# Performance work log

Hardware: AMD Instinct MI355X
Metric: run time of the kernel (lower is better)

Reference implementation:

```python
import jax, jax.numpy as jnp
import numpy as np
import math

T = 32
DIM = 1024
BATCH = 4096
ETA = 1.0


def setup_inputs() -> dict:
    key = jax.random.key(0)
    k1, k2, k3, k4 = jax.random.split(key, 4)
    x = jax.random.normal(k1, (BATCH, DIM), dtype=jnp.float32)
    mu = jax.random.uniform(k2, (T, DIM), dtype=jnp.float32, minval=-0.5, maxval=0.5)
    rho = jax.random.uniform(k3, (T, DIM), dtype=jnp.float32, minval=-0.5, maxval=0.5)
    # stochastic Beta(gamma_1, gamma_2) draws in the original (scipy beta.rvs);
    # passed as an explicit input, kept strictly inside (0, 1)
    beta_samples = jax.random.uniform(k4, (BATCH, T), dtype=jnp.float32,
                                      minval=0.01, maxval=0.99)
    return {"x": x, "mu": mu, "rho": rho, "beta_samples": beta_samples}


def _forward(x, mu, rho, beta_samples):
    B, D = x.shape
    Tn = mu.shape[0]
    log2pi = math.log(2.0 * math.pi)

    std = jnp.log1p(jnp.exp(rho))              # [T, D]
    log_std_sum = jnp.sum(jnp.log(std), axis=-1)   # [T]
    inv_var = 1.0 / (std * std)                # [T, D]

    # Diagonal Gaussian log-prob, batched over all T components via GEMMs
    quad = (jnp.einsum('bd,td->bt', x * x, inv_var)
            - 2.0 * jnp.einsum('bd,td->bt', x, mu * inv_var)
            + jnp.sum(mu * mu * inv_var, axis=-1)[None, :])   # [B, T]
    log_pdfs = -0.5 * D * log2pi - log_std_sum[None, :] - 0.5 * quad  # [B, T]

    # entropy of each diagonal Gaussian, broadcast to batch
    entropy = (D / 2.0) * (log2pi + 1.0) + log_std_sum   # [T]
    entropy = jnp.broadcast_to(entropy[None, :], (B, Tn))

    # stick-breaking weights: pi = mix_weights(beta)[:, :-1]
    beta1m_cumprod = jnp.cumprod(1.0 - beta_samples, axis=-1)   # [B, T]
    pi = beta_samples * jnp.concatenate(
        [jnp.ones((B, 1), x.dtype), beta1m_cumprod[:, :-1]], axis=-1)  # [B, T]
    log_pi = jnp.log(pi)

    # get_phi
    kl_gaussian = log_pdfs + entropy            # [B, T]
    N_t_gaussian = jnp.sum(kl_gaussian, axis=0, keepdims=True)  # [1, T]
    N_t_pi = jnp.sum(log_pi, axis=0, keepdims=True)             # [1, T]
    mix = N_t_pi / (N_t_gaussian + N_t_pi)      # [1, T]
    kl = mix * kl_gaussian + (1.0 - mix) * log_pi
    phi_new = jax.nn.softmax(kl, axis=1)        # [B, T]
    kl_g_mixed = mix * kl_gaussian              # [B, T]

    likelihood = jnp.mean(jnp.sum(phi_new * kl_g_mixed, axis=1), axis=0)  # scalar
    return likelihood


def reference(x, mu, rho, beta_samples):
    return _forward(x, mu, rho, beta_samples)
```

## Files before the change

kernel.cpp:

```cpp
#include <hip/hip_runtime.h>
#include <math.h>

constexpr int NT = 32;
constexpr int ND = 1024;
constexpr int NB = 4096;
constexpr int ROWS = 16;
constexpr int NBLK_MAIN = NB / ROWS;

typedef float f2 __attribute__((ext_vector_type(2)));

constexpr int OFF_M2C = 32768;
constexpr int OFF_C2  = 65536;
constexpr int OFF_KLG = 65600;
constexpr int OFF_LPI = 196672;
constexpr int OFF_PG  = 327744;
constexpr int OFF_PP  = 335936;

__global__ __launch_bounds__(256) void k_stats(const float* __restrict__ mu,
                                               const float* __restrict__ rho,
                                               float* __restrict__ ws,
                                               float* __restrict__ out) {
  float* ivc = ws;
  float* m2c = ws + OFF_M2C;
  float* c2  = ws + OFF_C2;

  const int t = blockIdx.x;
  const int c = threadIdx.x;

  float4 mu4  = reinterpret_cast<const float4*>(mu  + t * ND)[c];
  float4 rho4 = reinterpret_cast<const float4*>(rho + t * ND)[c];

  float rr[4] = {rho4.x, rho4.y, rho4.z, rho4.w};
  float mm[4] = {mu4.x,  mu4.y,  mu4.z,  mu4.w};
  float iv[4], m2[4];
  float c2p = 0.0f;
#pragma unroll
  for (int j = 0; j < 4; ++j) {
    float sd  = log1pf(expf(rr[j]));
    float ivv = 1.0f / (sd * sd);
    iv[j] = ivv;
    m2[j] = -2.0f * mm[j] * ivv;
    c2p  += mm[j] * mm[j] * ivv;
  }
  float4 iv4 = {iv[0], iv[1], iv[2], iv[3]};
  float4 m24 = {m2[0], m2[1], m2[2], m2[3]};
  reinterpret_cast<float4*>(ivc)[c * NT + t] = iv4;
  reinterpret_cast<float4*>(m2c)[c * NT + t] = m24;

#pragma unroll
  for (int m = 32; m >= 1; m >>= 1) c2p += __shfl_xor(c2p, m, 64);
  __shared__ float red[4];
  const int wave = threadIdx.x >> 6, lane = threadIdx.x & 63;
  if (lane == 0) red[wave] = c2p;
  __syncthreads();
  if (threadIdx.x == 0) {
    c2[t] = red[0] + red[1] + red[2] + red[3];
    if (t == 0) out[0] = 0.0f;
  }
}

__global__ __launch_bounds__(1024, 4) void k_main(const float* __restrict__ x,
                                                  const float* __restrict__ beta,
                                                  float* __restrict__ ws) {
  const float* ivc = ws;
  const float* m2c = ws + OFF_M2C;
  const float* c2  = ws + OFF_C2;
  float* klg = ws + OFF_KLG;
  float* lpi = ws + OFF_LPI;
  float* Pg  = ws + OFF_PG;
  float* Pp  = ws + OFF_PP;

  const int tid  = threadIdx.x;
  const int q    = tid >> 6;
  const int lane = tid & 63;
  const int h = lane >> 5, t = lane & 31;
  const int row0 = blockIdx.x * ROWS;

  __shared__ float xs[ROWS * ND];
  __shared__ float part[16][ROWS][32];

  {
    const float4* xg4 = reinterpret_cast<const float4*>(x) + (size_t)row0 * 256;
    float4* xs4w = reinterpret_cast<float4*>(xs);
#pragma unroll
    for (int k = 0; k < 4; ++k) {
      xs4w[k * 1024 + tid] = xg4[k * 1024 + tid];
    }
  }
  __syncthreads();

  const int c0 = q * 16 + h * 8;
  const float4* ivp = reinterpret_cast<const float4*>(ivc) + (size_t)c0 * NT + t;
  const float4* m2p = reinterpret_cast<const float4*>(m2c) + (size_t)c0 * NT + t;
  const float4* xs4 = reinterpret_cast<const float4*>(xs) + c0;

  f2 a2[ROWS];
#pragma unroll
  for (int r = 0; r < ROWS; ++r) a2[r] = (f2){0.f, 0.f};

#pragma unroll 1
  for (int i = 0; i < 8; ++i) {
    float4 iv4 = ivp[(size_t)i * NT];
    float4 m24 = m2p[(size_t)i * NT];
    const f2 ivl = {iv4.x, iv4.y}, ivh = {iv4.z, iv4.w};
    const f2 ml  = {m24.x, m24.y}, mh  = {m24.z, m24.w};
#pragma unroll
    for (int r = 0; r < ROWS; ++r) {
      float4 xv = xs4[r * 256 + i];
      const f2 xl = {xv.x, xv.y}, xh = {xv.z, xv.w};
      a2[r] = __builtin_elementwise_fma(xl, __builtin_elementwise_fma(xl, ivl, ml), a2[r]);
      a2[r] = __builtin_elementwise_fma(xh, __builtin_elementwise_fma(xh, ivh, mh), a2[r]);
    }
  }
#pragma unroll
  for (int r = 0; r < ROWS; ++r) {
    float s = a2[r].x + a2[r].y;
    s += __shfl_xor(s, 32, 64);
    if (h == 0) part[q][r][t] = s;
  }
  __syncthreads();

  const int rr = tid >> 5, t2 = tid & 31;
  float kv = 0.f, lp = 0.f;
  if (tid < 512) {
    float quad = 0.f;
#pragma unroll
    for (int w = 0; w < 16; ++w) quad += part[w][rr][t2];
    kv = 512.0f - 0.5f * (quad + c2[t2]);
    klg[(size_t)(row0 + rr) * NT + t2] = kv;

    const float b = beta[(size_t)(row0 + rr) * NT + t2];
    const float l1m = log1pf(-b);
    float s = l1m;
#pragma unroll
    for (int d = 1; d < 32; d <<= 1) {
      float v = __shfl_up(s, (unsigned)d, 32);
      if (t2 >= d) s += v;
    }
    lp = logf(b) + (s - l1m);
    lpi[(size_t)(row0 + rr) * NT + t2] = lp;
  }
  __syncthreads();
  if (tid < 512) {
    part[0][rr][t2] = kv;
    part[1][rr][t2] = lp;
  }
  __syncthreads();
  if (tid < 32) {
    float sg = 0.f, sp = 0.f;
#pragma unroll
    for (int r = 0; r < ROWS; ++r) { sg += part[0][r][tid]; sp += part[1][r][tid]; }
    Pg[(size_t)blockIdx.x * NT + tid] = sg;
    Pp[(size_t)blockIdx.x * NT + tid] = sp;
  }
}

__global__ __launch_bounds__(512) void k_final(const float* __restrict__ ws,
                                               float* __restrict__ out) {
  const float* klg = ws + OFF_KLG;
  const float* lpi = ws + OFF_LPI;
  const float* Pg  = ws + OFF_PG;
  const float* Pp  = ws + OFF_PP;

  const int tid  = threadIdx.x;
  const int wave = tid >> 6, lane = tid & 63;
  const int t = tid & 31;
  const int g = tid >> 5;

  __shared__ float ngF[32], npF[32];
  __shared__ float redG[8][32], redP[8][32];
  __shared__ float red[8];

  {
    float sg = 0.f, sp = 0.f;
#pragma unroll 4
    for (int b = g; b < NBLK_MAIN; b += 16) {
      sg += Pg[(size_t)b * NT + t];
      sp += Pp[(size_t)b * NT + t];
    }
    sg += __shfl_xor(sg, 32, 64);
    sp += __shfl_xor(sp, 32, 64);
    if (lane < 32) { redG[wave][t] = sg; redP[wave][t] = sp; }
  }
  __syncthreads();
  if (tid < 32) {
    float ng = 0.f, np = 0.f;
#pragma unroll
    for (int w = 0; w < 8; ++w) { ng += redG[w][tid]; np += redP[w][tid]; }
    ngF[tid] = ng;
    npF[tid] = np;
  }
  __syncthreads();

  const int row = blockIdx.x * 16 + g;
  const float kg = klg[(size_t)row * NT + t];
  const float lp = lpi[(size_t)row * NT + t];
  const float ng = ngF[t], np = npF[t];
  const float mix  = np / (ng + np);
  const float klgm = mix * kg;
  const float kl   = klgm + (1.0f - mix) * lp;

  float m = kl;
#pragma unroll
  for (int mk = 16; mk >= 1; mk >>= 1) m = fmaxf(m, __shfl_xor(m, mk, 64));
  const float e = expf(kl - m);
  float num = e * klgm, den = e;
#pragma unroll
  for (int mk = 16; mk >= 1; mk >>= 1) {
    num += __shfl_xor(num, mk, 64);
    den += __shfl_xor(den, mk, 64);
  }
  float s = num / den;
  s += __shfl_xor(s, 32, 64);

  if (lane == 0) red[wave] = s;
  __syncthreads();
  if (tid == 0) {
    float tot = 0.f;
#pragma unroll
    for (int w = 0; w < 8; ++w) tot += red[w];
    atomicAdd(out, tot * (1.0f / (float)NB));
  }
}

extern "C" void kernel_launch(void* const* d_in, const int* in_sizes, int n_in,
                              void* d_out, int out_size, void* d_ws, size_t ws_size,
                              hipStream_t stream) {
  const float* x    = (const float*)d_in[0];
  const float* mu   = (const float*)d_in[1];
  const float* rho  = (const float*)d_in[2];
  const float* beta = (const float*)d_in[3];
  float* out = (float*)d_out;
  float* ws  = (float*)d_ws;

  hipLaunchKernelGGL(k_stats, dim3(32),        dim3(256),  0, stream, mu, rho, ws, out);
  hipLaunchKernelGGL(k_main,  dim3(NBLK_MAIN), dim3(1024), 0, stream, x, beta, ws);
  hipLaunchKernelGGL(k_final, dim3(256),       dim3(512),  0, stream, ws, out);
}
```

Before: 29.63 us.

## Split main kernel rows into two tiles with register-staged prefetch of next tile

The main kernel now uses 512 threads and processes 16 rows as two 8-row tiles. The second tile's x data is loaded into registers while the first tile is computed, then written to a second shared buffer, so global loads overlap compute. Each wave now covers 32 columns instead of 16, giving fewer cross-wave partials but more serial work per thread. Per-tile partial sums double, so the final reduction reads twice as many partials. The extra barriers and the serialised epilogues between tiles may offset the overlap gain.

```diff
diff --git a/kernel.cpp b/kernel.cpp
--- a/kernel.cpp
+++ b/kernel.cpp
@@ -4,8 +4,10 @@
 constexpr int NT = 32;
 constexpr int ND = 1024;
 constexpr int NB = 4096;
-constexpr int ROWS = 16;
-constexpr int NBLK_MAIN = NB / ROWS;
+constexpr int TROWS = 8;
+constexpr int NTILE = 2;
+constexpr int NBLK_MAIN = NB / (TROWS * NTILE);
+constexpr int NPART = NB / TROWS;
 
 typedef float f2 __attribute__((ext_vector_type(2)));
 
@@ -14,7 +16,7 @@
 constexpr int OFF_KLG = 65600;
 constexpr int OFF_LPI = 196672;
 constexpr int OFF_PG  = 327744;
-constexpr int OFF_PP  = 335936;
+constexpr int OFF_PP  = 344128;
 
 __global__ __launch_bounds__(256) void k_stats(const float* __restrict__ mu,
                                                const float* __restrict__ rho,
@@ -59,9 +61,88 @@
   }
 }
 
-__global__ __launch_bounds__(1024, 4) void k_main(const float* __restrict__ x,
-                                                  const float* __restrict__ beta,
-                                                  float* __restrict__ ws) {
+__device__ __forceinline__ void compute_tile(const float* __restrict__ xsb,
+                                             const float* __restrict__ ivc,
+                                             const float* __restrict__ m2c,
+                                             float (*part)[8][32],
+                                             int q, int h, int t) {
+  const int c0 = q * 32 + h * 16;
+  const float4* ivp = reinterpret_cast<const float4*>(ivc) + (size_t)c0 * NT + t;
+  const float4* m2p = reinterpret_cast<const float4*>(m2c) + (size_t)c0 * NT + t;
+  const float4* xs4 = reinterpret_cast<const float4*>(xsb) + c0;
+
+  f2 a2[TROWS];
+#pragma unroll
+  for (int r = 0; r < TROWS; ++r) a2[r] = (f2){0.f, 0.f};
+
+#pragma unroll 4
+  for (int i = 0; i < 16; ++i) {
+    float4 iv4 = ivp[(size_t)i * NT];
+    float4 m24 = m2p[(size_t)i * NT];
+    const f2 ivl = {iv4.x, iv4.y}, ivh = {iv4.z, iv4.w};
+    const f2 ml  = {m24.x, m24.y}, mh  = {m24.z, m24.w};
+#pragma unroll
+    for (int r = 0; r < TROWS; ++r) {
+      float4 xv = xs4[r * 256 + i];
+      const f2 xl = {xv.x, xv.y}, xh = {xv.z, xv.w};
+      a2[r] = __builtin_elementwise_fma(xl, __builtin_elementwise_fma(xl, ivl, ml), a2[r]);
+      a2[r] = __builtin_elementwise_fma(xh, __builtin_elementwise_fma(xh, ivh, mh), a2[r]);
+    }
+  }
+#pragma unroll
+  for (int r = 0; r < TROWS; ++r) {
+    float s = a2[r].x + a2[r].y;
+    s += __shfl_xor(s, 32, 64);
+    if (h == 0) part[q][r][t] = s;
+  }
+}
+
+__device__ __forceinline__ void epilogue_tile(int tid, int rowB, int slot,
+                                              const float* __restrict__ beta,
+                                              const float* __restrict__ c2,
+                                              float (*part)[8][32],
+                                              float* __restrict__ klg,
+                                              float* __restrict__ lpi,
+                                              float* __restrict__ Pg,
+                                              float* __restrict__ Pp) {
+  const int rr = tid >> 5, t2 = tid & 31;
+  float kv = 0.f, lp = 0.f;
+  if (tid < 256) {
+    float quad = 0.f;
+#pragma unroll
+    for (int qq = 0; qq < 8; ++qq) quad += part[qq][rr][t2];
+    kv = 512.0f - 0.5f * (quad + c2[t2]);
+    klg[(size_t)(rowB + rr) * NT + t2] = kv;
+
+    const float b = beta[(size_t)(rowB + rr) * NT + t2];
+    const float l1m = log1pf(-b);
+    float s = l1m;
+#pragma unroll
+    for (int d = 1; d < 32; d <<= 1) {
+      float v = __shfl_up(s, (unsigned)d, 32);
+      if (t2 >= d) s += v;
+    }
+    lp = logf(b) + (s - l1m);
+    lpi[(size_t)(rowB + rr) * NT + t2] = lp;
+  }
+  __syncthreads();
+  if (tid < 256) {
+    part[0][rr][t2] = kv;
+    part[1][rr][t2] = lp;
+  }
+  __syncthreads();
+  if (tid < 32) {
+    float sg = 0.f, sp = 0.f;
+#pragma unroll
+    for (int r = 0; r < TROWS; ++r) { sg += part[0][r][tid]; sp += part[1][r][tid]; }
+    Pg[(size_t)slot * NT + tid] = sg;
+    Pp[(size_t)slot * NT + tid] = sp;
+  }
+}
+
+__global__ __launch_bounds__(512) void k_main(const float* __restrict__ x,
+                                              const float* __restrict__ beta,
+                                              float* __restrict__ ws) {
   const float* ivc = ws;
   const float* m2c = ws + OFF_M2C;
   const float* c2  = ws + OFF_C2;
@@ -74,85 +155,42 @@
   const int q    = tid >> 6;
   const int lane = tid & 63;
   const int h = lane >> 5, t = lane & 31;
-  const int row0 = blockIdx.x * ROWS;
-
-  __shared__ float xs[ROWS * ND];
-  __shared__ float part[16][ROWS][32];
-
+  const int row0 = blockIdx.x * (TROWS * NTILE);
+
+  __shared__ float xs0[TROWS * ND];
+  __shared__ float xs1[TROWS * ND];
+  __shared__ float part[8][TROWS][32];
+
+  const float4* xg4 = reinterpret_cast<const float4*>(x) + (size_t)row0 * 256;
+  float4 st[4];
+
+#pragma unroll
+  for (int k = 0; k < 4; ++k) st[k] = xg4[k * 512 + tid];
   {
-    const float4* xg4 = reinterpret_cast<const float4*>(x) + (size_t)row0 * 256;
-    float4* xs4w = reinterpret_cast<float4*>(xs);
-#pragma unroll
-    for (int k = 0; k < 4; ++k) {
-      xs4w[k * 1024 + tid] = xg4[k * 1024 + tid];
-    }
-  }
-  __syncthreads();
-
-  const int c0 = q * 16 + h * 8;
-  const float4* ivp = reinterpret_cast<const float4*>(ivc) + (size_t)c0 * NT + t;
-  const float4* m2p = reinterpret_cast<const float4*>(m2c) + (size_t)c0 * NT + t;
-  const float4* xs4 = reinterpret_cast<const float4*>(xs) + c0;
-
-  f2 a2[ROWS];
-#pragma unroll
-  for (int r = 0; r < ROWS; ++r) a2[r] = (f2){0.f, 0.f};
-
-#pragma unroll 1
-  for (int i = 0; i < 8; ++i) {
-    float4 iv4 = ivp[(size_t)i * NT];
-    float4 m24 = m2p[(size_t)i * NT];
-    const f2 ivl = {iv4.x, iv4.y}, ivh = {iv4.z, iv4.w};
-    const f2 ml  = {m24.x, m24.y}, mh  = {m24.z, m24.w};
-#pragma unroll
-    for (int r = 0; r < ROWS; ++r) {
-      float4 xv = xs4[r * 256 + i];
-      const f2 xl = {xv.x, xv.y}, xh = {xv.z, xv.w};
-      a2[r] = __builtin_elementwise_fma(xl, __builtin_elementwise_fma(xl, ivl, ml), a2[r]);
-      a2[r] = __builtin_elementwise_fma(xh, __builtin_elementwise_fma(xh, ivh, mh), a2[r]);
-    }
-  }
-#pragma unroll
-  for (int r = 0; r < ROWS; ++r) {
-    float s = a2[r].x + a2[r].y;
-    s += __shfl_xor(s, 32, 64);
-    if (h == 0) part[q][r][t] = s;
-  }
-  __syncthreads();
-
-  const int rr = tid >> 5, t2 = tid & 31;
-  float kv = 0.f, lp = 0.f;
-  if (tid < 512) {
-    float quad = 0.f;
-#pragma unroll
-    for (int w = 0; w < 16; ++w) quad += part[w][rr][t2];
-    kv = 512.0f - 0.5f * (quad + c2[t2]);
-    klg[(size_t)(row0 + rr) * NT + t2] = kv;
-
-    const float b = beta[(size_t)(row0 + rr) * NT + t2];
-    const float l1m = log1pf(-b);
-    float s = l1m;
-#pragma unroll
-    for (int d = 1; d < 32; d <<= 1) {
-      float v = __shfl_up(s, (unsigned)d, 32);
-      if (t2 >= d) s += v;
-    }
-    lp = logf(b) + (s - l1m);
-    lpi[(size_t)(row0 + rr) * NT + t2] = lp;
-  }
-  __syncthreads();
-  if (tid < 512) {
-    part[0][rr][t2] = kv;
-    part[1][rr][t2] = lp;
-  }
-  __syncthreads();
-  if (tid < 32) {
-    float sg = 0.f, sp = 0.f;
-#pragma unroll
-    for (int r = 0; r < ROWS; ++r) { sg += part[0][r][tid]; sp += part[1][r][tid]; }
-    Pg[(size_t)blockIdx.x * NT + tid] = sg;
-    Pp[(size_t)blockIdx.x * NT + tid] = sp;
-  }
+    float4* w = reinterpret_cast<float4*>(xs0);
+#pragma unroll
+    for (int k = 0; k < 4; ++k) w[k * 512 + tid] = st[k];
+  }
+  __syncthreads();
+
+#pragma unroll
+  for (int k = 0; k < 4; ++k) st[k] = xg4[2048 + k * 512 + tid];
+
+  compute_tile(xs0, ivc, m2c, part, q, h, t);
+
+  {
+    float4* w = reinterpret_cast<float4*>(xs1);
+#pragma unroll
+    for (int k = 0; k < 4; ++k) w[k * 512 + tid] = st[k];
+  }
+  __syncthreads();
+
+  epilogue_tile(tid, row0, blockIdx.x * 2 + 0, beta, c2, part, klg, lpi, Pg, Pp);
+  __syncthreads();
+
+  compute_tile(xs1, ivc, m2c, part, q, h, t);
+  __syncthreads();
+  epilogue_tile(tid, row0 + TROWS, blockIdx.x * 2 + 1, beta, c2, part, klg, lpi, Pg, Pp);
 }
 
 __global__ __launch_bounds__(512) void k_final(const float* __restrict__ ws,
@@ -173,8 +211,8 @@
 
   {
     float sg = 0.f, sp = 0.f;
-#pragma unroll 4
-    for (int b = g; b < NBLK_MAIN; b += 16) {
+#pragma unroll 8
+    for (int b = g; b < NPART; b += 16) {
       sg += Pg[(size_t)b * NT + t];
       sp += Pp[(size_t)b * NT + t];
     }
@@ -233,7 +271,7 @@
   float* out = (float*)d_out;
   float* ws  = (float*)d_ws;
 
-  hipLaunchKernelGGL(k_stats, dim3(32),        dim3(256),  0, stream, mu, rho, ws, out);
-  hipLaunchKernelGGL(k_main,  dim3(NBLK_MAIN), dim3(1024), 0, stream, x, beta, ws);
-  hipLaunchKernelGGL(k_final, dim3(256),       dim3(512),  0, stream, ws, out);
-}
+  hipLaunchKernelGGL(k_stats, dim3(32),        dim3(256), 0, stream, mu, rho, ws, out);
+  hipLaunchKernelGGL(k_main,  dim3(NBLK_MAIN), dim3(512), 0, stream, x, beta, ws);
+  hipLaunchKernelGGL(k_final, dim3(256),       dim3(512), 0, stream, ws, out);
+}
```

Measured after the change: 38.97 us. 1.32x slower.
